# Kernel tuning notes

Hardware: AMD Instinct MI355X
Metric: run time of the kernel (lower is better)

The kernel has to match this reference:

```python
import jax, jax.numpy as jnp
import numpy as np

B, S, DIM = 4, 4096, 1024
H, HD = 16, 64  # n_heads, head_dim = dim // n_heads
UMV = 20.0      # unified_max_value (init kwarg)


def setup_inputs() -> dict:
    key = jax.random.key(0)
    kx, kw = jax.random.split(key)
    x = jax.random.normal(kx, (B, S, DIM), dtype=jnp.float32)
    # qkv_proj: Linear(dim, 3*dim). Small weight scale + positive bias keeps
    # attention scores inside the keep-window [0, 2*UMV] so denominators are safe.
    W_qkv = jax.random.normal(kw, (DIM, 3 * DIM), dtype=jnp.float32) * 0.02
    b_qkv = jnp.full((3 * DIM,), 0.5, dtype=jnp.float32)
    return {"x": x, "W_qkv": W_qkv, "b_qkv": b_qkv}


def reference(x, W_qkv, b_qkv):
    Bb, Ss, _ = x.shape
    qkv = x @ W_qkv + b_qkv                      # [B,S,3*dim]
    qkv = qkv.reshape(Bb, Ss, H, 3 * HD)          # [B,S,H,3*hd]
    Q, K, V = jnp.split(qkv, 3, axis=-1)          # each [B,S,H,hd]
    # matmul(Q, K.transpose(-2,-1)) on [B,S,H,hd]: contract head_dim -> [B,S,H,H]
    s = jnp.einsum('bshd,bsgd->bshg', Q, K) - UMV
    e = jnp.exp(s)
    mask = (s > UMV) | (s < -UMV)                 # keep only s in [-UMV, UMV]
    e = jnp.where(mask, 0.0, e)
    denom = jnp.sum(e, axis=-1, keepdims=True)
    p = e / denom                                  # [B,S,H,H]
    out = jnp.einsum('bshg,bsgd->bshd', p, V)      # [B,S,H,hd]
    return out
```

## Files before the change

### kernel.cpp

```cpp
#include <hip/hip_runtime.h>

typedef _Float16 v8h __attribute__((ext_vector_type(8)));
typedef _Float16 v4h __attribute__((ext_vector_type(4)));
typedef _Float16 v2h __attribute__((ext_vector_type(2)));
typedef float v4f __attribute__((ext_vector_type(4)));

__device__ __forceinline__ void gl16(const void* g, void* l) {
    __builtin_amdgcn_global_load_lds(
        (const __attribute__((address_space(1))) unsigned int*)g,
        (__attribute__((address_space(3))) unsigned int*)l, 16, 0, 0);
}

__device__ __forceinline__ void wave_lds_fence() {
    asm volatile("s_waitcnt lgkmcnt(0)" ::: "memory");
}

__global__ __launch_bounds__(256) void k_cvt(const float* __restrict__ x,
                                             _Float16* __restrict__ x16,
                                             const float* __restrict__ W,
                                             _Float16* __restrict__ Wt) {
    if (blockIdx.x < 8192) {
        int i = (blockIdx.x * 256 + threadIdx.x) * 8;
        float4 a = *(const float4*)(x + i);
        float4 b = *(const float4*)(x + i + 4);
        v8h h;
        h[0] = (_Float16)a.x; h[1] = (_Float16)a.y; h[2] = (_Float16)a.z; h[3] = (_Float16)a.w;
        h[4] = (_Float16)b.x; h[5] = (_Float16)b.y; h[6] = (_Float16)b.z; h[7] = (_Float16)b.w;
        *(v8h*)(x16 + i) = h;
    } else {
        __shared__ float T[64][68];
        int bid = blockIdx.x - 8192;
        int k0 = (bid & 15) * 64;
        int n0 = (bid >> 4) * 64;
        int t = threadIdx.x;
        int tr = t >> 4;
        int tc = t & 15;
#pragma unroll
        for (int rr = 0; rr < 4; rr++) {
            int kk = rr * 16 + tr;
            float4 v = *(const float4*)(W + (size_t)(k0 + kk) * 3072 + n0 + tc * 4);
            T[kk][tc * 4 + 0] = v.x; T[kk][tc * 4 + 1] = v.y;
            T[kk][tc * 4 + 2] = v.z; T[kk][tc * 4 + 3] = v.w;
        }
        __syncthreads();
#pragma unroll
        for (int ww = 0; ww < 4; ww++) {
            int nn = ww * 16 + tr;
            v4h h;
#pragma unroll
            for (int i = 0; i < 4; i++) h[i] = (_Float16)T[tc * 4 + i][nn];
            *(v4h*)(Wt + (size_t)(n0 + nn) * 1024 + k0 + tc * 4) = h;
        }
    }
}

__global__ __launch_bounds__(256) void k_gemm(const _Float16* __restrict__ A,
                                              const _Float16* __restrict__ Bt,
                                              const float* __restrict__ bias,
                                              _Float16* __restrict__ C) {
    __shared__ __align__(16) _Float16 As[128 * 32];
    __shared__ __align__(16) _Float16 Bs[128 * 32];
    int bm = blockIdx.x & 127;
    int bn = blockIdx.x >> 7;
    int m0 = bm * 128, n0 = bn * 128;
    int tid = threadIdx.x;
    int w = tid >> 6, lane = tid & 63;
    int quad = lane >> 4, l15 = lane & 15;
    int wm = (w & 1) * 64, wn = (w >> 1) * 64;

    int mc1 = w * 16 + (lane >> 2);
    int mc2 = (w + 4) * 16 + (lane >> 2);
    int k8 = (lane & 3) * 8;
    const _Float16* aS1 = A + (size_t)(m0 + mc1) * 1024 + k8;
    const _Float16* aS2 = A + (size_t)(m0 + mc2) * 1024 + k8;
    const _Float16* bS1 = Bt + (size_t)(n0 + mc1) * 1024 + k8;
    const _Float16* bS2 = Bt + (size_t)(n0 + mc2) * 1024 + k8;
    _Float16* lA1 = &As[w * 512];
    _Float16* lA2 = &As[(w + 4) * 512];
    _Float16* lB1 = &Bs[w * 512];
    _Float16* lB2 = &Bs[(w + 4) * 512];

    v4f acc[4][4] = {};

    for (int kt = 0; kt < 1024; kt += 32) {
        __syncthreads();
        gl16(aS1 + kt, lA1);
        gl16(aS2 + kt, lA2);
        gl16(bS1 + kt, lB1);
        gl16(bS2 + kt, lB2);
        __syncthreads();
        v8h af[4], bf[4];
#pragma unroll
        for (int mi = 0; mi < 4; mi++)
            af[mi] = *(const v8h*)&As[(wm + mi * 16 + l15) * 32 + quad * 8];
#pragma unroll
        for (int ni = 0; ni < 4; ni++)
            bf[ni] = *(const v8h*)&Bs[(wn + ni * 16 + l15) * 32 + quad * 8];
#pragma unroll
        for (int mi = 0; mi < 4; mi++)
#pragma unroll
            for (int ni = 0; ni < 4; ni++)
                acc[mi][ni] = __builtin_amdgcn_mfma_f32_16x16x32_f16(af[mi], bf[ni], acc[mi][ni], 0, 0, 0);
    }

#pragma unroll
    for (int ni = 0; ni < 4; ni++) {
        int n = n0 + wn + ni * 16 + l15;
        float bv = bias[n];
#pragma unroll
        for (int mi = 0; mi < 4; mi++) {
            int mbase = m0 + wm + mi * 16 + quad * 4;
#pragma unroll
            for (int r = 0; r < 4; r++)
                C[(size_t)(mbase + r) * 3072 + n] = (_Float16)(acc[mi][ni][r] + bv);
        }
    }
}

__global__ __launch_bounds__(256) void k_attn(const _Float16* __restrict__ qkv,
                                              float* __restrict__ out) {
    __shared__ __align__(16) _Float16 Lh[4][16 * 200];
    __shared__ float Pb[4][16 * 17];
    int tid = threadIdx.x;
    int w = tid >> 6, lane = tid & 63;
    int pos = blockIdx.x * 4 + w;
    _Float16* L = Lh[w];
    float* P = Pb[w];
    const _Float16* src = qkv + (size_t)pos * 3072;

#pragma unroll
    for (int ii = 0; ii < 6; ii++) {
        int e = (ii * 64 + lane) * 8;
        v8h v = *(const v8h*)(src + e);
        int h = e / 192, r = e % 192;
        *(v8h*)(L + h * 200 + r) = v;
    }
    wave_lds_fence();

    {
        int h = lane & 15, quad = lane >> 4;
        const _Float16* Qr = L + h * 200;
        v8h q[8];
#pragma unroll
        for (int d = 0; d < 8; d++) q[d] = *(const v8h*)(Qr + d * 8);
        float e4[4];
#pragma unroll
        for (int c = 0; c < 4; c++) {
            const _Float16* Kr = L + (quad * 4 + c) * 200 + 64;
            float a = 0.f;
#pragma unroll
            for (int d = 0; d < 8; d++) {
                v8h k = *(const v8h*)(Kr + d * 8);
#pragma unroll
                for (int j = 0; j < 4; j++)
                    a = __builtin_amdgcn_fdot2(((v2h*)&q[d])[j], ((v2h*)&k)[j], a, false);
            }
            float s = a - 20.0f;
            e4[c] = (s > 20.0f || s < -20.0f) ? 0.0f : __expf(s);
        }
        float part = e4[0] + e4[1] + e4[2] + e4[3];
        part += __shfl_xor(part, 16, 64);
        part += __shfl_xor(part, 32, 64);
        float inv = 1.0f / part;
#pragma unroll
        for (int c = 0; c < 4; c++) P[h * 17 + quad * 4 + c] = e4[c] * inv;
    }
    wave_lds_fence();

    {
        int h2 = lane >> 2, db = (lane & 3) * 16;
        v2h o2[8] = {};
#pragma unroll
        for (int g = 0; g < 16; g++) {
            _Float16 ph = (_Float16)P[h2 * 17 + g];
            v2h p2; p2[0] = ph; p2[1] = ph;
            const _Float16* Vr = L + g * 200 + 128 + db;
            v8h v0 = *(const v8h*)(Vr);
            v8h v1 = *(const v8h*)(Vr + 8);
#pragma unroll
            for (int j = 0; j < 4; j++) {
                o2[j]     = p2 * ((v2h*)&v0)[j] + o2[j];
                o2[4 + j] = p2 * ((v2h*)&v1)[j] + o2[4 + j];
            }
        }
        float* dst = out + (size_t)pos * 1024 + h2 * 64 + db;
#pragma unroll
        for (int d4 = 0; d4 < 4; d4++) {
            float4 v;
            v.x = (float)o2[d4 * 2][0];
            v.y = (float)o2[d4 * 2][1];
            v.z = (float)o2[d4 * 2 + 1][0];
            v.w = (float)o2[d4 * 2 + 1][1];
            *(float4*)(dst + d4 * 4) = v;
        }
    }
}

extern "C" void kernel_launch(void* const* d_in, const int* in_sizes, int n_in,
                              void* d_out, int out_size, void* d_ws, size_t ws_size,
                              hipStream_t stream) {
    (void)in_sizes; (void)n_in; (void)out_size; (void)ws_size;
    const float* x  = (const float*)d_in[0];
    const float* Wq = (const float*)d_in[1];
    const float* bq = (const float*)d_in[2];
    float* out = (float*)d_out;

    char* ws = (char*)d_ws;
    _Float16* x16   = (_Float16*)ws;
    _Float16* wt16  = (_Float16*)(ws + (32u << 20));
    _Float16* qkv16 = (_Float16*)(ws + (38u << 20));

    k_cvt<<<8960, 256, 0, stream>>>(x, x16, Wq, wt16);
    k_gemm<<<3072, 256, 0, stream>>>(x16, wt16, bq, qkv16);
    k_attn<<<4096, 256, 0, stream>>>(qkv16, out);
}
```

Measured before the change: 291.0 us.

## Compute per-position head scores with MFMA and stage fp16 buffers in output

Replaces the per-lane fdot2 loops for the 16x16 head-score matrix with two 16x16x32 MFMA instructions, and switches the row-sum reduction to shuffles within 16-lane groups to match the MFMA output layout. It also relocates the fp16 x and transposed-weight scratch buffers into the output buffer, with qkv placed at the start of the workspace. That reuse is safe only because the attention kernel overwrites the output afterwards. The intent is to cut ALU work in the attention kernel and possibly improve memory locality, at the cost of extra shuffles per row.

```diff
diff --git a/kernel.cpp b/kernel.cpp
--- a/kernel.cpp
+++ b/kernel.cpp
@@ -137,33 +137,31 @@
     }
     wave_lds_fence();
 
+    int l15 = lane & 15, quad = lane >> 4;
     {
-        int h = lane & 15, quad = lane >> 4;
-        const _Float16* Qr = L + h * 200;
-        v8h q[8];
-#pragma unroll
-        for (int d = 0; d < 8; d++) q[d] = *(const v8h*)(Qr + d * 8);
+        const _Float16* row = L + l15 * 200;
+        v8h a0 = *(const v8h*)(row + quad * 8);
+        v8h a1 = *(const v8h*)(row + 32 + quad * 8);
+        v8h b0 = *(const v8h*)(row + 64 + quad * 8);
+        v8h b1 = *(const v8h*)(row + 96 + quad * 8);
+        v4f s = {};
+        s = __builtin_amdgcn_mfma_f32_16x16x32_f16(a0, b0, s, 0, 0, 0);
+        s = __builtin_amdgcn_mfma_f32_16x16x32_f16(a1, b1, s, 0, 0, 0);
         float e4[4];
 #pragma unroll
-        for (int c = 0; c < 4; c++) {
-            const _Float16* Kr = L + (quad * 4 + c) * 200 + 64;
-            float a = 0.f;
-#pragma unroll
-            for (int d = 0; d < 8; d++) {
-                v8h k = *(const v8h*)(Kr + d * 8);
-#pragma unroll
-                for (int j = 0; j < 4; j++)
-                    a = __builtin_amdgcn_fdot2(((v2h*)&q[d])[j], ((v2h*)&k)[j], a, false);
-            }
-            float s = a - 20.0f;
-            e4[c] = (s > 20.0f || s < -20.0f) ? 0.0f : __expf(s);
-        }
-        float part = e4[0] + e4[1] + e4[2] + e4[3];
-        part += __shfl_xor(part, 16, 64);
-        part += __shfl_xor(part, 32, 64);
-        float inv = 1.0f / part;
-#pragma unroll
-        for (int c = 0; c < 4; c++) P[h * 17 + quad * 4 + c] = e4[c] * inv;
+        for (int r = 0; r < 4; r++) {
+            float sv = s[r] - 20.0f;
+            e4[r] = (sv > 20.0f || sv < -20.0f) ? 0.0f : __expf(sv);
+        }
+#pragma unroll
+        for (int r = 0; r < 4; r++) {
+            float t = e4[r];
+            t += __shfl_xor(t, 1, 64);
+            t += __shfl_xor(t, 2, 64);
+            t += __shfl_xor(t, 4, 64);
+            t += __shfl_xor(t, 8, 64);
+            P[(quad * 4 + r) * 17 + l15] = e4[r] / t;
+        }
     }
     wave_lds_fence();
 
@@ -205,10 +203,10 @@
     const float* bq = (const float*)d_in[2];
     float* out = (float*)d_out;
 
-    char* ws = (char*)d_ws;
-    _Float16* x16   = (_Float16*)ws;
-    _Float16* wt16  = (_Float16*)(ws + (32u << 20));
-    _Float16* qkv16 = (_Float16*)(ws + (38u << 20));
+    char* ob = (char*)d_out;
+    _Float16* x16   = (_Float16*)ob;
+    _Float16* wt16  = (_Float16*)(ob + (48u << 20));
+    _Float16* qkv16 = (_Float16*)d_ws;
 
     k_cvt<<<8960, 256, 0, stream>>>(x, x16, Wq, wt16);
     k_gemm<<<3072, 256, 0, stream>>>(x16, wt16, bq, qkv16);
```

Result: no change. 289.9 us (-0.4%).
